# Kernel optimization log

Measured on AMD Instinct MI355X. Metric: run time of the kernel, lower is better.

The kernel has to match this reference:

```python
import jax, jax.numpy as jnp
import numpy as np
import math

B, WIN, C_IN, C_OUT = 8, 512, 38, 38
D_MODEL, N_HEADS, E_LAYERS, D_FF = 512, 8, 3, 512
EH = D_MODEL // N_HEADS
LN_EPS = 1e-3  # keras LayerNormalization default


def setup_inputs() -> dict:
    key = jax.random.key(0)
    ks = jax.random.split(key, 24)
    s = 0.02
    rn = lambda k, sh: jax.random.normal(k, sh, jnp.float32) * s
    L, d, H = E_LAYERS, D_MODEL, N_HEADS
    return {
        "x": jax.random.normal(ks[0], (B, WIN, C_IN), jnp.float32),
        "conv_k": rn(ks[1], (3, C_IN, d)),
        "Wq": rn(ks[2], (L, d, d)), "bq": jnp.zeros((L, d), jnp.float32),
        "Wk": rn(ks[3], (L, d, d)), "bk": jnp.zeros((L, d), jnp.float32),
        "Wv": rn(ks[4], (L, d, d)), "bv": jnp.zeros((L, d), jnp.float32),
        "Ws": rn(ks[5], (L, d, H)), "bs": jnp.zeros((L, H), jnp.float32),
        "Wo": rn(ks[6], (L, d, d)), "bo": jnp.zeros((L, d), jnp.float32),
        "W1": rn(ks[7], (L, d, D_FF)), "b1": jnp.zeros((L, D_FF), jnp.float32),
        "W2": rn(ks[8], (L, D_FF, d)), "b2": jnp.zeros((L, d), jnp.float32),
        "ln1_g": jnp.ones((L, d), jnp.float32), "ln1_b": jnp.zeros((L, d), jnp.float32),
        "ln2_g": jnp.ones((L, d), jnp.float32), "ln2_b": jnp.zeros((L, d), jnp.float32),
        "lnf_g": jnp.ones((d,), jnp.float32), "lnf_b": jnp.zeros((d,), jnp.float32),
        "Wp": rn(ks[9], (d, C_OUT)), "bp": jnp.zeros((C_OUT,), jnp.float32),
    }


def _layernorm(x, g, b):
    mu = jnp.mean(x, axis=-1, keepdims=True)
    var = jnp.mean((x - mu) ** 2, axis=-1, keepdims=True)
    return (x - mu) * jax.lax.rsqrt(var + LN_EPS) * g + b


def _pos_embedding():
    pos = jnp.arange(WIN, dtype=jnp.float32)[:, None]
    div = jnp.exp(jnp.arange(0, D_MODEL, 2, dtype=jnp.float32) * (-math.log(10000.0) / D_MODEL))
    # interleave sin at even idx, cos at odd idx
    return jnp.stack([jnp.sin(pos * div), jnp.cos(pos * div)], axis=-1).reshape(WIN, D_MODEL)


def reference(x, conv_k, Wq, bq, Wk, bk, Wv, bv, Ws, bs, Wo, bo,
              W1, b1, W2, b2, ln1_g, ln1_b, ln2_g, ln2_b, lnf_g, lnf_b, Wp, bp):
    # --- DataEmbedding: wrap-pad then Conv1D(k=3, valid), plus sinusoidal PE ---
    xp = jnp.concatenate([x[:, -1:], x, x[:, :1]], axis=1)
    h = jax.lax.conv_general_dilated(xp, conv_k, window_strides=(1,), padding='VALID',
                                     dimension_numbers=('NWC', 'WIO', 'NWC'))
    h = h + _pos_embedding()[None]

    idx = jnp.arange(WIN, dtype=jnp.float32)
    dist = jnp.abs(idx[:, None] - idx[None, :])
    scale = 1.0 / math.sqrt(EH)
    inv_sqrt_2pi = 1.0 / math.sqrt(2.0 * math.pi)

    series_l, prior_l, sigma_l = [], [], []
    for i in range(E_LAYERS):
        q = (h @ Wq[i] + bq[i]).reshape(B, WIN, N_HEADS, EH)
        k = (h @ Wk[i] + bk[i]).reshape(B, WIN, N_HEADS, EH)
        v = (h @ Wv[i] + bv[i]).reshape(B, WIN, N_HEADS, EH)
        sig = h @ Ws[i] + bs[i]

        scores = jnp.einsum('blhe,bshe->bhls', q, k)  # mask_flag=False in model
        series = jax.nn.softmax(scores * scale, axis=-1)  # [B, H, L, S]

        sg = jnp.transpose(sig, (0, 2, 1))               # [B, H, L]
        sg = jax.nn.sigmoid(sg * 5.0) + 1e-5
        sg = jnp.power(3.0, sg) - 1.0
        sg4 = jnp.broadcast_to(sg[..., None], (B, N_HEADS, WIN, WIN))
        prior = inv_sqrt_2pi / sg4 * jnp.exp(-(dist ** 2) / (2.0 * sg4 ** 2))

        attn_out = jnp.einsum('bhls,bshd->blhd', series, v).reshape(B, WIN, D_MODEL)
        h = _layernorm(h + attn_out @ Wo[i] + bo[i], ln1_g[i], ln1_b[i])
        y = jax.nn.gelu(h @ W1[i] + b1[i], approximate=False)
        y = y @ W2[i] + b2[i]
        h = _layernorm(h + y, ln2_g[i], ln2_b[i])

        series_l.append(series); prior_l.append(prior); sigma_l.append(sg4)

    h = _layernorm(h, lnf_g, lnf_b)
    out = h @ Wp + bp
    return (out, jnp.stack(series_l), jnp.stack(prior_l), jnp.stack(sigma_l))
```

## Files before the change

kernel.cpp:

```cpp
#include <hip/hip_runtime.h>
#include <math.h>


typedef unsigned short ushort;
typedef __attribute__((ext_vector_type(8))) ushort ushort8;
typedef __attribute__((ext_vector_type(8))) short short8;
typedef __attribute__((ext_vector_type(4))) float float4v;

__device__ inline ushort f2bf(float f) {
  union { float f; unsigned u; } v; v.f = f;
  return (ushort)((v.u + 0x7fffu + ((v.u >> 16) & 1u)) >> 16);
}

__global__ __launch_bounds__(512) void embed_kernel(const float* __restrict__ x,
                                                    const float* __restrict__ ck,
                                                    float* __restrict__ h) {
  int bt = blockIdx.x;
  int b = bt >> 9, t = bt & 511;
  int co = threadIdx.x;
  __shared__ float xs[3][38];
  if (co < 114) {
    int w = co / 38, ci = co - w * 38;
    int r = (t - 1 + w + 512) & 511;
    xs[w][ci] = x[((long)(b << 9) + r) * 38 + ci];
  }
  __syncthreads();
  float acc = 0.f;
#pragma unroll
  for (int w = 0; w < 3; ++w)
#pragma unroll
    for (int ci = 0; ci < 38; ++ci)
      acc = fmaf(xs[w][ci], ck[(w * 38 + ci) * 512 + co], acc);
  float div = expf((float)(co & ~1) * (-9.210340371976184f / 512.f));
  float ang = (float)t * div;
  float pe = (co & 1) ? cosf(ang) : sinf(ang);
  h[(long)bt * 512 + co] = acc + pe;
}

__global__ __launch_bounds__(256) void wcvt_kernel(const float* __restrict__ W,
                                                   ushort* __restrict__ Wt) {
  int l = blockIdx.z;
  int n = blockIdx.x * 256 + threadIdx.x;
  int k0 = blockIdx.y * 8;
  const float* w = W + (long)l * 262144;
  ushort* o = Wt + (long)l * 262144;
  ushort8 v;
#pragma unroll
  for (int i = 0; i < 8; ++i) v[i] = f2bf(w[(long)(k0 + i) * 512 + n]);
  *(ushort8*)&o[(long)n * 512 + k0] = v;
}

template <bool ABF16, bool BKMAJOR, bool GELU_, bool CBF16>
__global__ __launch_bounds__(256) void gemm_mfma(
    const void* __restrict__ Av, int lda, long sA1, long sA2,
    const ushort* __restrict__ B, int ldb, long sB1, long sB2,
    const float* __restrict__ bias,
    void* __restrict__ Cv, int ldc, long sC1, long sC2,
    int K, int bdiv, float alpha) {
  int z = blockIdx.z;
  int z1 = z / bdiv, z2 = z - z1 * bdiv;
  long aoff = (long)z1 * sA1 + (long)z2 * sA2;
  B += (long)z1 * sB1 + (long)z2 * sB2;
  long coff = (long)z1 * sC1 + (long)z2 * sC2;

  __shared__ ushort As[64 * 40];
  __shared__ ushort Bs[64 * 40];
  int t = threadIdx.x;
  int m0 = blockIdx.y * 64, n0 = blockIdx.x * 64;
  int w = t >> 6, lane = t & 63;
  int wr = (w >> 1) * 32, wc = (w & 1) * 32;
  int fm = lane & 15, koff = (lane >> 4) * 8;

  float4v acc[2][2] = {{{0.f, 0.f, 0.f, 0.f}, {0.f, 0.f, 0.f, 0.f}},
                       {{0.f, 0.f, 0.f, 0.f}, {0.f, 0.f, 0.f, 0.f}}};

  int sm = t >> 2, skq = (t & 3) * 8;
  int bk = t >> 3, bnq = (t & 7) * 8;

  for (int k0 = 0; k0 < K; k0 += 32) {
    if (ABF16) {
      const ushort* Ab = (const ushort*)Av + aoff;
      *(ushort8*)&As[sm * 40 + skq] =
          *(const ushort8*)&Ab[(long)(m0 + sm) * lda + k0 + skq];
    } else {
      const float* Af = (const float*)Av + aoff;
      const float* ap = &Af[(long)(m0 + sm) * lda + k0 + skq];
      float4 x0 = *(const float4*)ap;
      float4 x1 = *(const float4*)(ap + 4);
      ushort8 v;
      v[0] = f2bf(x0.x); v[1] = f2bf(x0.y); v[2] = f2bf(x0.z); v[3] = f2bf(x0.w);
      v[4] = f2bf(x1.x); v[5] = f2bf(x1.y); v[6] = f2bf(x1.z); v[7] = f2bf(x1.w);
      *(ushort8*)&As[sm * 40 + skq] = v;
    }
    if (!BKMAJOR) {
      *(ushort8*)&Bs[sm * 40 + skq] =
          *(const ushort8*)&B[(long)(n0 + sm) * ldb + k0 + skq];
    } else {
      ushort8 v = *(const ushort8*)&B[(long)(k0 + bk) * ldb + n0 + bnq];
#pragma unroll
      for (int i = 0; i < 8; ++i) Bs[(bnq + i) * 40 + bk] = v[i];
    }
    __syncthreads();

    short8 a0 = *(const short8*)&As[(wr + fm) * 40 + koff];
    short8 a1 = *(const short8*)&As[(wr + 16 + fm) * 40 + koff];
    short8 b0 = *(const short8*)&Bs[(wc + fm) * 40 + koff];
    short8 b1 = *(const short8*)&Bs[(wc + 16 + fm) * 40 + koff];
    acc[0][0] = __builtin_amdgcn_mfma_f32_16x16x32_bf16(a0, b0, acc[0][0], 0, 0, 0);
    acc[0][1] = __builtin_amdgcn_mfma_f32_16x16x32_bf16(a0, b1, acc[0][1], 0, 0, 0);
    acc[1][0] = __builtin_amdgcn_mfma_f32_16x16x32_bf16(a1, b0, acc[1][0], 0, 0, 0);
    acc[1][1] = __builtin_amdgcn_mfma_f32_16x16x32_bf16(a1, b1, acc[1][1], 0, 0, 0);
    __syncthreads();
  }

#pragma unroll
  for (int j = 0; j < 2; ++j) {
    int col = n0 + wc + 16 * j + fm;
    float bv = bias ? bias[col] : 0.f;
#pragma unroll
    for (int i = 0; i < 2; ++i) {
#pragma unroll
      for (int r = 0; r < 4; ++r) {
        int row = m0 + wr + 16 * i + (lane >> 4) * 4 + r;
        float v = acc[i][j][r] * alpha + bv;
        if (GELU_) v = 0.5f * v * (1.f + erff(v * 0.7071067811865476f));
        if (CBF16)
          ((ushort*)Cv)[coff + (long)row * ldc + col] = f2bf(v);
        else
          ((float*)Cv)[coff + (long)row * ldc + col] = v;
      }
    }
  }
}

__global__ __launch_bounds__(256) void softmax_kernel(float* __restrict__ P) {
  long row = (long)blockIdx.x * 4 + (threadIdx.x >> 6);
  int lane = threadIdx.x & 63;
  float* p = P + row * 512 + lane * 8;
  float4 v0 = *(float4*)p;
  float4 v1 = *(float4*)(p + 4);
  float m = fmaxf(fmaxf(fmaxf(v0.x, v0.y), fmaxf(v0.z, v0.w)),
                  fmaxf(fmaxf(v1.x, v1.y), fmaxf(v1.z, v1.w)));
#pragma unroll
  for (int off = 1; off < 64; off <<= 1) m = fmaxf(m, __shfl_xor(m, off));
  v0.x = __expf(v0.x - m); v0.y = __expf(v0.y - m);
  v0.z = __expf(v0.z - m); v0.w = __expf(v0.w - m);
  v1.x = __expf(v1.x - m); v1.y = __expf(v1.y - m);
  v1.z = __expf(v1.z - m); v1.w = __expf(v1.w - m);
  float s = v0.x + v0.y + v0.z + v0.w + v1.x + v1.y + v1.z + v1.w;
#pragma unroll
  for (int off = 1; off < 64; off <<= 1) s += __shfl_xor(s, off);
  float inv = 1.f / s;
  v0.x *= inv; v0.y *= inv; v0.z *= inv; v0.w *= inv;
  v1.x *= inv; v1.y *= inv; v1.z *= inv; v1.w *= inv;
  *(float4*)p = v0;
  *(float4*)(p + 4) = v1;
}

__global__ __launch_bounds__(256) void prior_kernel(const float* __restrict__ sig,
                                                    float* __restrict__ prior,
                                                    float* __restrict__ sigma4) {
  int blk = blockIdx.x;
  int i = blk & 511;
  int bh = blk >> 9;
  int b = bh >> 3, hh = bh & 7;
  float xv = sig[(((long)b << 9) + i) * 8 + hh];
  float s = 1.f / (1.f + expf(-5.f * xv)) + 1e-5f;
  float sg = expm1f(s * 1.0986122886681098f);
  float inv = 0.3989422804014327f / sg;
  float rinv = 1.f / sg;
  long base = ((long)bh << 18) + ((long)i << 9);
  int j0 = threadIdx.x * 2;
  float d0 = fabsf((float)(i - j0));
  float d1 = fabsf((float)(i - (j0 + 1)));
  float r0 = d0 * rinv, r1 = d1 * rinv;
  float2 pv = {inv * expf(-0.5f * r0 * r0), inv * expf(-0.5f * r1 * r1)};
  float2 sv = {sg, sg};
  *(float2*)&prior[base + j0] = pv;
  *(float2*)&sigma4[base + j0] = sv;
}

__global__ __launch_bounds__(256) void ln_kernel(const float* __restrict__ x,
                                                 const float* __restrict__ delta,
                                                 const float* __restrict__ g,
                                                 const float* __restrict__ bb,
                                                 float* __restrict__ out) {
  long row = blockIdx.x;
  int tid = threadIdx.x;
  int c = tid * 2;
  float2 xv = *(const float2*)&x[row * 512 + c];
  if (delta) {
    float2 dv = *(const float2*)&delta[row * 512 + c];
    xv.x += dv.x; xv.y += dv.y;
  }
  float s = xv.x + xv.y;
  float q = xv.x * xv.x + xv.y * xv.y;
#pragma unroll
  for (int off = 1; off < 64; off <<= 1) {
    s += __shfl_xor(s, off);
    q += __shfl_xor(q, off);
  }
  __shared__ float red[8];
  int wid = tid >> 6;
  if ((tid & 63) == 0) { red[wid] = s; red[wid + 4] = q; }
  __syncthreads();
  float S = red[0] + red[1] + red[2] + red[3];
  float Q = red[4] + red[5] + red[6] + red[7];
  float mean = S * (1.f / 512.f);
  float var = Q * (1.f / 512.f) - mean * mean;
  float rstd = rsqrtf(var + 1e-3f);
  float2 o;
  o.x = (xv.x - mean) * rstd * g[c] + bb[c];
  o.y = (xv.y - mean) * rstd * g[c + 1] + bb[c + 1];
  *(float2*)&out[row * 512 + c] = o;
}

template <int NOUT>
__global__ __launch_bounds__(256) void gemm_smallN(const float* __restrict__ A,
                                                   const float* __restrict__ W,
                                                   const float* __restrict__ bias,
                                                   float* __restrict__ C) {
  long row = (long)blockIdx.x * 4 + (threadIdx.x >> 6);
  int lane = threadIdx.x & 63;
  float acc[NOUT];
#pragma unroll
  for (int j = 0; j < NOUT; ++j) acc[j] = 0.f;
  for (int k = lane; k < 512; k += 64) {
    float a = A[row * 512 + k];
    const float* wr = W + (long)k * NOUT;
#pragma unroll
    for (int j = 0; j < NOUT; ++j) acc[j] = fmaf(a, wr[j], acc[j]);
  }
#pragma unroll
  for (int j = 0; j < NOUT; ++j)
#pragma unroll
    for (int off = 32; off; off >>= 1) acc[j] += __shfl_xor(acc[j], off);
  if (lane == 0) {
#pragma unroll
    for (int j = 0; j < NOUT; ++j) C[row * NOUT + j] = acc[j] + bias[j];
  }
}

extern "C" void kernel_launch(void* const* d_in, const int* in_sizes, int n_in,
                              void* d_out, int out_size, void* d_ws, size_t ws_size,
                              hipStream_t stream) {
  (void)in_sizes; (void)n_in; (void)out_size; (void)ws_size;
  const float* x    = (const float*)d_in[0];
  const float* ck   = (const float*)d_in[1];
  const float* Wq   = (const float*)d_in[2];
  const float* bq   = (const float*)d_in[3];
  const float* Wk   = (const float*)d_in[4];
  const float* bk   = (const float*)d_in[5];
  const float* Wv   = (const float*)d_in[6];
  const float* bv   = (const float*)d_in[7];
  const float* Wsw  = (const float*)d_in[8];
  const float* bsw  = (const float*)d_in[9];
  const float* Wo   = (const float*)d_in[10];
  const float* bo   = (const float*)d_in[11];
  const float* W1   = (const float*)d_in[12];
  const float* b1   = (const float*)d_in[13];
  const float* W2   = (const float*)d_in[14];
  const float* b2   = (const float*)d_in[15];
  const float* ln1g = (const float*)d_in[16];
  const float* ln1b = (const float*)d_in[17];
  const float* ln2g = (const float*)d_in[18];
  const float* ln2b = (const float*)d_in[19];
  const float* lnfg = (const float*)d_in[20];
  const float* lnfb = (const float*)d_in[21];
  const float* Wp   = (const float*)d_in[22];
  const float* bp   = (const float*)d_in[23];
  float* out = (float*)d_out;

  float* h  = (float*)d_ws;
  float* t1 = h + 2097152;
  float* t2 = t1 + 2097152;
  float* sg = t2 + 2097152;
  ushort* qb = (ushort*)(sg + 32768);
  ushort* kb = qb + 2097152;
  ushort* vb = kb + 2097152;
  ushort* wt = vb + 2097152;

  float* series0 = out + 155648;
  float* prior0  = out + 50487296;
  float* sigma0  = out + 100818944;

  dim3 gW(2, 64, 3);
  wcvt_kernel<<<gW, 256, 0, stream>>>(Wq, wt + 0L * 3 * 262144);
  wcvt_kernel<<<gW, 256, 0, stream>>>(Wk, wt + 1L * 3 * 262144);
  wcvt_kernel<<<gW, 256, 0, stream>>>(Wv, wt + 2L * 3 * 262144);
  wcvt_kernel<<<gW, 256, 0, stream>>>(Wo, wt + 3L * 3 * 262144);
  wcvt_kernel<<<gW, 256, 0, stream>>>(W1, wt + 4L * 3 * 262144);
  wcvt_kernel<<<gW, 256, 0, stream>>>(W2, wt + 5L * 3 * 262144);

  embed_kernel<<<4096, 512, 0, stream>>>(x, ck, h);

  dim3 gFull(8, 64, 1);
  dim3 gScore(8, 8, 64);
  dim3 gAttn(1, 8, 64);

  for (int l = 0; l < 3; ++l) {
    const ushort* wtq = wt + (0L * 3 + l) * 262144;
    const ushort* wtk = wt + (1L * 3 + l) * 262144;
    const ushort* wtv = wt + (2L * 3 + l) * 262144;
    const ushort* wto = wt + (3L * 3 + l) * 262144;
    const ushort* wt1 = wt + (4L * 3 + l) * 262144;
    const ushort* wt2 = wt + (5L * 3 + l) * 262144;
    const float* Ws_l = Wsw + (long)l * 4096;  const float* bs_l = bsw + (long)l * 8;
    float* ser = series0 + (long)l * 16777216;
    float* pri = prior0  + (long)l * 16777216;
    float* sgm = sigma0  + (long)l * 16777216;

    gemm_mfma<false, false, false, true><<<gFull, 256, 0, stream>>>(
        h, 512, 0, 0, wtq, 512, 0, 0, bq + (long)l * 512, qb, 512, 0, 0, 512, 1, 1.f);
    gemm_mfma<false, false, false, true><<<gFull, 256, 0, stream>>>(
        h, 512, 0, 0, wtk, 512, 0, 0, bk + (long)l * 512, kb, 512, 0, 0, 512, 1, 1.f);
    gemm_mfma<false, false, false, true><<<gFull, 256, 0, stream>>>(
        h, 512, 0, 0, wtv, 512, 0, 0, bv + (long)l * 512, vb, 512, 0, 0, 512, 1, 1.f);
    gemm_smallN<8><<<1024, 256, 0, stream>>>(h, Ws_l, bs_l, sg);
    gemm_mfma<true, false, false, false><<<gScore, 256, 0, stream>>>(
        qb, 512, 262144, 64, kb, 512, 262144, 64, nullptr,
        ser, 512, 2097152, 262144, 64, 8, 0.125f);
    softmax_kernel<<<8192, 256, 0, stream>>>(ser);
    prior_kernel<<<32768, 256, 0, stream>>>(sg, pri, sgm);
    gemm_mfma<false, true, false, false><<<gAttn, 256, 0, stream>>>(
        ser, 512, 2097152, 262144, vb, 512, 262144, 64, nullptr,
        t1, 512, 262144, 64, 512, 8, 1.f);
    gemm_mfma<false, false, false, false><<<gFull, 256, 0, stream>>>(
        t1, 512, 0, 0, wto, 512, 0, 0, bo + (long)l * 512, t2, 512, 0, 0, 512, 1, 1.f);
    ln_kernel<<<4096, 256, 0, stream>>>(h, t2, ln1g + l * 512, ln1b + l * 512, h);
    gemm_mfma<false, false, true, false><<<gFull, 256, 0, stream>>>(
        h, 512, 0, 0, wt1, 512, 0, 0, b1 + (long)l * 512, t1, 512, 0, 0, 512, 1, 1.f);
    gemm_mfma<false, false, false, false><<<gFull, 256, 0, stream>>>(
        t1, 512, 0, 0, wt2, 512, 0, 0, b2 + (long)l * 512, t2, 512, 0, 0, 512, 1, 1.f);
    ln_kernel<<<4096, 256, 0, stream>>>(h, t2, ln2g + l * 512, ln2b + l * 512, h);
  }

  ln_kernel<<<4096, 256, 0, stream>>>(h, nullptr, lnfg, lnfb, t1);
  gemm_smallN<38><<<1024, 256, 0, stream>>>(t1, Wp, bp, out);
}
```

Baseline: 1.244 ms.

## Fuse attention scores, softmax, PV and prior into one kernel; merge QKV GEMMs

Q, K and V projections now run as a single GEMM with concatenated weights and biases, writing an interleaved bf16 QKV buffer. A new fused attention kernel per 64-row tile and head computes scores with MFMA, does the row softmax in registers with cross-wave reductions, writes series, keeps the probabilities in LDS as bf16 for the PV product, and also writes prior and sigma. This removes the separate score, softmax, PV and prior launches and the re-reading of the large series matrix from global memory. The cost is heavy LDS use and a high register count at occupancy 1, and a serialized in-block prior write loop.

```diff
diff --git a/kernel.cpp b/kernel.cpp
--- a/kernel.cpp
+++ b/kernel.cpp
@@ -38,31 +38,36 @@
 }
 
 __global__ __launch_bounds__(256) void wcvt_kernel(const float* __restrict__ W,
-                                                   ushort* __restrict__ Wt) {
+                                                   ushort* __restrict__ Wt,
+                                                   long lstride) {
   int l = blockIdx.z;
   int n = blockIdx.x * 256 + threadIdx.x;
   int k0 = blockIdx.y * 8;
   const float* w = W + (long)l * 262144;
-  ushort* o = Wt + (long)l * 262144;
+  ushort* o = Wt + (long)l * lstride;
   ushort8 v;
 #pragma unroll
   for (int i = 0; i < 8; ++i) v[i] = f2bf(w[(long)(k0 + i) * 512 + n]);
   *(ushort8*)&o[(long)n * 512 + k0] = v;
 }
 
-template <bool ABF16, bool BKMAJOR, bool GELU_, bool CBF16>
+__global__ __launch_bounds__(512) void bcat_kernel(const float* __restrict__ bq,
+                                                   const float* __restrict__ bk,
+                                                   const float* __restrict__ bv,
+                                                   float* __restrict__ bqkv) {
+  int l = blockIdx.x, t = threadIdx.x;
+  bqkv[l * 1536 + t] = bq[l * 512 + t];
+  bqkv[l * 1536 + 512 + t] = bk[l * 512 + t];
+  bqkv[l * 1536 + 1024 + t] = bv[l * 512 + t];
+}
+
+template <bool ABF16, bool GELU_, bool CBF16>
 __global__ __launch_bounds__(256) void gemm_mfma(
-    const void* __restrict__ Av, int lda, long sA1, long sA2,
-    const ushort* __restrict__ B, int ldb, long sB1, long sB2,
+    const void* __restrict__ Av, int lda,
+    const ushort* __restrict__ B, int ldb,
     const float* __restrict__ bias,
-    void* __restrict__ Cv, int ldc, long sC1, long sC2,
-    int K, int bdiv, float alpha) {
-  int z = blockIdx.z;
-  int z1 = z / bdiv, z2 = z - z1 * bdiv;
-  long aoff = (long)z1 * sA1 + (long)z2 * sA2;
-  B += (long)z1 * sB1 + (long)z2 * sB2;
-  long coff = (long)z1 * sC1 + (long)z2 * sC2;
-
+    void* __restrict__ Cv, int ldc,
+    int K, float alpha) {
   __shared__ ushort As[64 * 40];
   __shared__ ushort Bs[64 * 40];
   int t = threadIdx.x;
@@ -73,17 +78,15 @@
 
   float4v acc[2][2] = {{{0.f, 0.f, 0.f, 0.f}, {0.f, 0.f, 0.f, 0.f}},
                        {{0.f, 0.f, 0.f, 0.f}, {0.f, 0.f, 0.f, 0.f}}};
-
   int sm = t >> 2, skq = (t & 3) * 8;
-  int bk = t >> 3, bnq = (t & 7) * 8;
 
   for (int k0 = 0; k0 < K; k0 += 32) {
     if (ABF16) {
-      const ushort* Ab = (const ushort*)Av + aoff;
+      const ushort* Ab = (const ushort*)Av;
       *(ushort8*)&As[sm * 40 + skq] =
           *(const ushort8*)&Ab[(long)(m0 + sm) * lda + k0 + skq];
     } else {
-      const float* Af = (const float*)Av + aoff;
+      const float* Af = (const float*)Av;
       const float* ap = &Af[(long)(m0 + sm) * lda + k0 + skq];
       float4 x0 = *(const float4*)ap;
       float4 x1 = *(const float4*)(ap + 4);
@@ -92,14 +95,8 @@
       v[4] = f2bf(x1.x); v[5] = f2bf(x1.y); v[6] = f2bf(x1.z); v[7] = f2bf(x1.w);
       *(ushort8*)&As[sm * 40 + skq] = v;
     }
-    if (!BKMAJOR) {
-      *(ushort8*)&Bs[sm * 40 + skq] =
-          *(const ushort8*)&B[(long)(n0 + sm) * ldb + k0 + skq];
-    } else {
-      ushort8 v = *(const ushort8*)&B[(long)(k0 + bk) * ldb + n0 + bnq];
-#pragma unroll
-      for (int i = 0; i < 8; ++i) Bs[(bnq + i) * 40 + bk] = v[i];
-    }
+    *(ushort8*)&Bs[sm * 40 + skq] =
+        *(const ushort8*)&B[(long)(n0 + sm) * ldb + k0 + skq];
     __syncthreads();
 
     short8 a0 = *(const short8*)&As[(wr + fm) * 40 + koff];
@@ -125,59 +122,213 @@
         float v = acc[i][j][r] * alpha + bv;
         if (GELU_) v = 0.5f * v * (1.f + erff(v * 0.7071067811865476f));
         if (CBF16)
-          ((ushort*)Cv)[coff + (long)row * ldc + col] = f2bf(v);
+          ((ushort*)Cv)[(long)row * ldc + col] = f2bf(v);
         else
-          ((float*)Cv)[coff + (long)row * ldc + col] = v;
+          ((float*)Cv)[(long)row * ldc + col] = v;
       }
     }
   }
 }
 
-__global__ __launch_bounds__(256) void softmax_kernel(float* __restrict__ P) {
-  long row = (long)blockIdx.x * 4 + (threadIdx.x >> 6);
-  int lane = threadIdx.x & 63;
-  float* p = P + row * 512 + lane * 8;
-  float4 v0 = *(float4*)p;
-  float4 v1 = *(float4*)(p + 4);
-  float m = fmaxf(fmaxf(fmaxf(v0.x, v0.y), fmaxf(v0.z, v0.w)),
-                  fmaxf(fmaxf(v1.x, v1.y), fmaxf(v1.z, v1.w)));
-#pragma unroll
-  for (int off = 1; off < 64; off <<= 1) m = fmaxf(m, __shfl_xor(m, off));
-  v0.x = __expf(v0.x - m); v0.y = __expf(v0.y - m);
-  v0.z = __expf(v0.z - m); v0.w = __expf(v0.w - m);
-  v1.x = __expf(v1.x - m); v1.y = __expf(v1.y - m);
-  v1.z = __expf(v1.z - m); v1.w = __expf(v1.w - m);
-  float s = v0.x + v0.y + v0.z + v0.w + v1.x + v1.y + v1.z + v1.w;
-#pragma unroll
-  for (int off = 1; off < 64; off <<= 1) s += __shfl_xor(s, off);
-  float inv = 1.f / s;
-  v0.x *= inv; v0.y *= inv; v0.z *= inv; v0.w *= inv;
-  v1.x *= inv; v1.y *= inv; v1.z *= inv; v1.w *= inv;
-  *(float4*)p = v0;
-  *(float4*)(p + 4) = v1;
-}
-
-__global__ __launch_bounds__(256) void prior_kernel(const float* __restrict__ sig,
-                                                    float* __restrict__ prior,
-                                                    float* __restrict__ sigma4) {
-  int blk = blockIdx.x;
-  int i = blk & 511;
-  int bh = blk >> 9;
+__global__ __launch_bounds__(256, 1) void attn_fused(
+    const ushort* __restrict__ qkv, const float* __restrict__ sg,
+    float* __restrict__ series, float* __restrict__ prior,
+    float* __restrict__ sigma, float* __restrict__ t1) {
+  __shared__ ushort KPs[36864];
+  __shared__ ushort Qs[4608];
+  __shared__ ushort Vc[4608];
+  __shared__ float red[256];
+
+  int t = threadIdx.x;
+  int m0 = blockIdx.x * 64;
+  int bh = blockIdx.y;
   int b = bh >> 3, hh = bh & 7;
-  float xv = sig[(((long)b << 9) + i) * 8 + hh];
-  float s = 1.f / (1.f + expf(-5.f * xv)) + 1e-5f;
-  float sg = expm1f(s * 1.0986122886681098f);
-  float inv = 0.3989422804014327f / sg;
-  float rinv = 1.f / sg;
-  long base = ((long)bh << 18) + ((long)i << 9);
-  int j0 = threadIdx.x * 2;
-  float d0 = fabsf((float)(i - j0));
-  float d1 = fabsf((float)(i - (j0 + 1)));
-  float r0 = d0 * rinv, r1 = d1 * rinv;
-  float2 pv = {inv * expf(-0.5f * r0 * r0), inv * expf(-0.5f * r1 * r1)};
-  float2 sv = {sg, sg};
-  *(float2*)&prior[base + j0] = pv;
-  *(float2*)&sigma4[base + j0] = sv;
+  int w = t >> 6, lane = t & 63;
+  int fm = lane & 15, q4 = lane >> 4;
+  int wc = w * 128;
+  long rowg = (long)b * 512;
+
+  {
+    int row = t >> 2, kq = (t & 3) * 16;
+    const ushort* src = &qkv[(rowg + m0 + row) * 1536 + hh * 64 + kq];
+    *(ushort8*)&Qs[row * 72 + kq] = *(const ushort8*)src;
+    *(ushort8*)&Qs[row * 72 + kq + 8] = *(const ushort8*)(src + 8);
+#pragma unroll
+    for (int p = 0; p < 8; ++p) {
+      int srow = p * 64 + row;
+      const ushort* ks = &qkv[(rowg + srow) * 1536 + 512 + hh * 64 + kq];
+      *(ushort8*)&KPs[srow * 72 + kq] = *(const ushort8*)ks;
+      *(ushort8*)&KPs[srow * 72 + kq + 8] = *(const ushort8*)(ks + 8);
+    }
+  }
+  __syncthreads();
+
+  float4v acc[4][8];
+#pragma unroll
+  for (int i = 0; i < 4; ++i)
+#pragma unroll
+    for (int j = 0; j < 8; ++j) acc[i][j] = (float4v){0.f, 0.f, 0.f, 0.f};
+
+#pragma unroll
+  for (int ks = 0; ks < 2; ++ks) {
+    int ko = ks * 32 + q4 * 8;
+    short8 a[4], bfr[8];
+#pragma unroll
+    for (int i = 0; i < 4; ++i)
+      a[i] = *(const short8*)&Qs[(16 * i + fm) * 72 + ko];
+#pragma unroll
+    for (int j = 0; j < 8; ++j)
+      bfr[j] = *(const short8*)&KPs[(wc + 16 * j + fm) * 72 + ko];
+#pragma unroll
+    for (int i = 0; i < 4; ++i)
+#pragma unroll
+      for (int j = 0; j < 8; ++j)
+        acc[i][j] = __builtin_amdgcn_mfma_f32_16x16x32_bf16(a[i], bfr[j], acc[i][j], 0, 0, 0);
+  }
+
+#pragma unroll
+  for (int i = 0; i < 4; ++i)
+#pragma unroll
+    for (int j = 0; j < 8; ++j)
+#pragma unroll
+      for (int r = 0; r < 4; ++r) acc[i][j][r] *= 0.125f;
+
+  float mrow[4][4];
+#pragma unroll
+  for (int i = 0; i < 4; ++i)
+#pragma unroll
+    for (int r = 0; r < 4; ++r) {
+      float m = acc[i][0][r];
+#pragma unroll
+      for (int j = 1; j < 8; ++j) m = fmaxf(m, acc[i][j][r]);
+#pragma unroll
+      for (int off = 1; off < 16; off <<= 1) m = fmaxf(m, __shfl_xor(m, off));
+      mrow[i][r] = m;
+    }
+  if (fm == 0) {
+#pragma unroll
+    for (int i = 0; i < 4; ++i)
+#pragma unroll
+      for (int r = 0; r < 4; ++r)
+        red[(16 * i + q4 * 4 + r) * 4 + w] = mrow[i][r];
+  }
+  __syncthreads();
+#pragma unroll
+  for (int i = 0; i < 4; ++i)
+#pragma unroll
+    for (int r = 0; r < 4; ++r) {
+      const float* rp = &red[(16 * i + q4 * 4 + r) * 4];
+      mrow[i][r] = fmaxf(fmaxf(rp[0], rp[1]), fmaxf(rp[2], rp[3]));
+    }
+  float lrow[4][4];
+#pragma unroll
+  for (int i = 0; i < 4; ++i)
+#pragma unroll
+    for (int r = 0; r < 4; ++r) {
+      float s = 0.f;
+#pragma unroll
+      for (int j = 0; j < 8; ++j) {
+        float e = __expf(acc[i][j][r] - mrow[i][r]);
+        acc[i][j][r] = e;
+        s += e;
+      }
+#pragma unroll
+      for (int off = 1; off < 16; off <<= 1) s += __shfl_xor(s, off);
+      lrow[i][r] = s;
+    }
+  __syncthreads();
+  if (fm == 0) {
+#pragma unroll
+    for (int i = 0; i < 4; ++i)
+#pragma unroll
+      for (int r = 0; r < 4; ++r)
+        red[(16 * i + q4 * 4 + r) * 4 + w] = lrow[i][r];
+  }
+  __syncthreads();
+#pragma unroll
+  for (int i = 0; i < 4; ++i)
+#pragma unroll
+    for (int r = 0; r < 4; ++r) {
+      const float* rp = &red[(16 * i + q4 * 4 + r) * 4];
+      lrow[i][r] = 1.f / (rp[0] + rp[1] + rp[2] + rp[3]);
+    }
+
+  float* serp = series + ((long)bh << 18);
+#pragma unroll
+  for (int i = 0; i < 4; ++i)
+#pragma unroll
+    for (int r = 0; r < 4; ++r) {
+      int row = 16 * i + q4 * 4 + r;
+      float inv = lrow[i][r];
+#pragma unroll
+      for (int j = 0; j < 8; ++j) {
+        int col = wc + 16 * j + fm;
+        float v = acc[i][j][r] * inv;
+        serp[(long)(m0 + row) * 512 + col] = v;
+        KPs[row * 520 + col] = f2bf(v);
+      }
+    }
+
+  float4v acc2[4] = {{0.f, 0.f, 0.f, 0.f}, {0.f, 0.f, 0.f, 0.f},
+                     {0.f, 0.f, 0.f, 0.f}, {0.f, 0.f, 0.f, 0.f}};
+  int wn = w * 16;
+  int s_local = t >> 2, cgrp = (t & 3) * 16;
+  for (int c = 0; c < 8; ++c) {
+    __syncthreads();
+    const ushort* vs = &qkv[(rowg + c * 64 + s_local) * 1536 + 1024 + hh * 64 + cgrp];
+    ushort8 v0 = *(const ushort8*)vs;
+    ushort8 v1 = *(const ushort8*)(vs + 8);
+#pragma unroll
+    for (int e = 0; e < 8; ++e) {
+      Vc[(cgrp + e) * 72 + s_local] = v0[e];
+      Vc[(cgrp + 8 + e) * 72 + s_local] = v1[e];
+    }
+    __syncthreads();
+#pragma unroll
+    for (int ks = 0; ks < 2; ++ks) {
+      int ko = ks * 32 + q4 * 8;
+      short8 b2 = *(const short8*)&Vc[(wn + fm) * 72 + ko];
+#pragma unroll
+      for (int i = 0; i < 4; ++i) {
+        short8 a2 = *(const short8*)&KPs[(16 * i + fm) * 520 + c * 64 + ko];
+        acc2[i] = __builtin_amdgcn_mfma_f32_16x16x32_bf16(a2, b2, acc2[i], 0, 0, 0);
+      }
+    }
+  }
+#pragma unroll
+  for (int i = 0; i < 4; ++i)
+#pragma unroll
+    for (int r = 0; r < 4; ++r)
+      t1[(rowg + m0 + 16 * i + q4 * 4 + r) * 512 + hh * 64 + wn + fm] = acc2[i][r];
+
+  __syncthreads();
+  if (t < 64) {
+    float xv = sg[(rowg + m0 + t) * 8 + hh];
+    float s = 1.f / (1.f + __expf(-5.f * xv)) + 1e-5f;
+    float sgv = expm1f(s * 1.0986122886681098f);
+    red[t * 3] = sgv;
+    red[t * 3 + 1] = 0.3989422804014327f / sgv;
+    red[t * 3 + 2] = 1.f / sgv;
+  }
+  __syncthreads();
+  float* prip = prior + ((long)bh << 18);
+  float* sigp = sigma + ((long)bh << 18);
+  for (int it = t; it < 8192; it += 256) {
+    int row = it >> 7;
+    int c4 = (it & 127) << 2;
+    float sgv = red[row * 3], inv = red[row * 3 + 1], rinv = red[row * 3 + 2];
+    float ig = (float)(m0 + row);
+    float4 pv, sv;
+#pragma unroll
+    for (int e = 0; e < 4; ++e) {
+      float dd = ig - (float)(c4 + e);
+      float rr = dd * rinv;
+      ((float*)&pv)[e] = inv * __expf(-0.5f * rr * rr);
+      ((float*)&sv)[e] = sgv;
+    }
+    *(float4*)&prip[(long)(m0 + row) * 512 + c4] = pv;
+    *(float4*)&sigp[(long)(m0 + row) * 512 + c4] = sv;
+  }
 }
 
 __global__ __launch_bounds__(256) void ln_kernel(const float* __restrict__ x,
@@ -271,67 +422,52 @@
   const float* bp   = (const float*)d_in[23];
   float* out = (float*)d_out;
 
-  float* h  = (float*)d_ws;
-  float* t1 = h + 2097152;
-  float* t2 = t1 + 2097152;
-  float* sg = t2 + 2097152;
-  ushort* qb = (ushort*)(sg + 32768);
-  ushort* kb = qb + 2097152;
-  ushort* vb = kb + 2097152;
-  ushort* wt = vb + 2097152;
+  float* h    = (float*)d_ws;
+  float* t1   = h + 2097152;
+  float* t2   = t1 + 2097152;
+  float* sg   = t2 + 2097152;
+  float* bqkv = sg + 32768;
+  ushort* qkv  = (ushort*)(bqkv + 4608);
+  ushort* wqkv = qkv + 6291456;
+  ushort* wo3  = wqkv + 2359296;
+  ushort* w13  = wo3 + 786432;
+  ushort* w23  = w13 + 786432;
 
   float* series0 = out + 155648;
   float* prior0  = out + 50487296;
   float* sigma0  = out + 100818944;
 
   dim3 gW(2, 64, 3);
-  wcvt_kernel<<<gW, 256, 0, stream>>>(Wq, wt + 0L * 3 * 262144);
-  wcvt_kernel<<<gW, 256, 0, stream>>>(Wk, wt + 1L * 3 * 262144);
-  wcvt_kernel<<<gW, 256, 0, stream>>>(Wv, wt + 2L * 3 * 262144);
-  wcvt_kernel<<<gW, 256, 0, stream>>>(Wo, wt + 3L * 3 * 262144);
-  wcvt_kernel<<<gW, 256, 0, stream>>>(W1, wt + 4L * 3 * 262144);
-  wcvt_kernel<<<gW, 256, 0, stream>>>(W2, wt + 5L * 3 * 262144);
+  wcvt_kernel<<<gW, 256, 0, stream>>>(Wq, wqkv, 786432);
+  wcvt_kernel<<<gW, 256, 0, stream>>>(Wk, wqkv + 262144, 786432);
+  wcvt_kernel<<<gW, 256, 0, stream>>>(Wv, wqkv + 524288, 786432);
+  wcvt_kernel<<<gW, 256, 0, stream>>>(Wo, wo3, 262144);
+  wcvt_kernel<<<gW, 256, 0, stream>>>(W1, w13, 262144);
+  wcvt_kernel<<<gW, 256, 0, stream>>>(W2, w23, 262144);
+  bcat_kernel<<<3, 512, 0, stream>>>(bq, bk, bv, bqkv);
 
   embed_kernel<<<4096, 512, 0, stream>>>(x, ck, h);
 
+  dim3 gQKV(24, 64, 1);
   dim3 gFull(8, 64, 1);
-  dim3 gScore(8, 8, 64);
-  dim3 gAttn(1, 8, 64);
+  dim3 gAttn(8, 64, 1);
 
   for (int l = 0; l < 3; ++l) {
-    const ushort* wtq = wt + (0L * 3 + l) * 262144;
-    const ushort* wtk = wt + (1L * 3 + l) * 262144;
-    const ushort* wtv = wt + (2L * 3 + l) * 262144;
-    const ushort* wto = wt + (3L * 3 + l) * 262144;
-    const ushort* wt1 = wt + (4L * 3 + l) * 262144;
-    const ushort* wt2 = wt + (5L * 3 + l) * 262144;
-    const float* Ws_l = Wsw + (long)l * 4096;  const float* bs_l = bsw + (long)l * 8;
     float* ser = series0 + (long)l * 16777216;
     float* pri = prior0  + (long)l * 16777216;
     float* sgm = sigma0  + (long)l * 16777216;
 
-    gemm_mfma<false, false, false, true><<<gFull, 256, 0, stream>>>(
-        h, 512, 0, 0, wtq, 512, 0, 0, bq + (long)l * 512, qb, 512, 0, 0, 512, 1, 1.f);
-    gemm_mfma<false, false, false, true><<<gFull, 256, 0, stream>>>(
-        h, 512, 0, 0, wtk, 512, 0, 0, bk + (long)l * 512, kb, 512, 0, 0, 512, 1, 1.f);
-    gemm_mfma<false, false, false, true><<<gFull, 256, 0, stream>>>(
-        h, 512, 0, 0, wtv, 512, 0, 0, bv + (long)l * 512, vb, 512, 0, 0, 512, 1, 1.f);
-    gemm_smallN<8><<<1024, 256, 0, stream>>>(h, Ws_l, bs_l, sg);
-    gemm_mfma<true, false, false, false><<<gScore, 256, 0, stream>>>(
-        qb, 512, 262144, 64, kb, 512, 262144, 64, nullptr,
-        ser, 512, 2097152, 262144, 64, 8, 0.125f);
-    softmax_kernel<<<8192, 256, 0, stream>>>(ser);
-    prior_kernel<<<32768, 256, 0, stream>>>(sg, pri, sgm);
-    gemm_mfma<false, true, false, false><<<gAttn, 256, 0, stream>>>(
-        ser, 512, 2097152, 262144, vb, 512, 262144, 64, nullptr,
-        t1, 512, 262144, 64, 512, 8, 1.f);
-    gemm_mfma<false, false, false, false><<<gFull, 256, 0, stream>>>(
-        t1, 512, 0, 0, wto, 512, 0, 0, bo + (long)l * 512, t2, 512, 0, 0, 512, 1, 1.f);
+    gemm_mfma<false, false, true><<<gQKV, 256, 0, stream>>>(
+        h, 512, wqkv + (long)l * 786432, 512, bqkv + l * 1536, qkv, 1536, 512, 1.f);
+    gemm_smallN<8><<<1024, 256, 0, stream>>>(h, Wsw + (long)l * 4096, bsw + l * 8, sg);
+    attn_fused<<<gAttn, 256, 0, stream>>>(qkv, sg, ser, pri, sgm, t1);
+    gemm_mfma<false, false, false><<<gFull, 256, 0, stream>>>(
+        t1, 512, wo3 + (long)l * 262144, 512, bo + (long)l * 512, t2, 512, 512, 1.f);
     ln_kernel<<<4096, 256, 0, stream>>>(h, t2, ln1g + l * 512, ln1b + l * 512, h);
-    gemm_mfma<false, false, true, false><<<gFull, 256, 0, stream>>>(
-        h, 512, 0, 0, wt1, 512, 0, 0, b1 + (long)l * 512, t1, 512, 0, 0, 512, 1, 1.f);
-    gemm_mfma<false, false, false, false><<<gFull, 256, 0, stream>>>(
-        t1, 512, 0, 0, wt2, 512, 0, 0, b2 + (long)l * 512, t2, 512, 0, 0, 512, 1, 1.f);
+    gemm_mfma<false, true, false><<<gFull, 256, 0, stream>>>(
+        h, 512, w13 + (long)l * 262144, 512, b1 + (long)l * 512, t1, 512, 512, 1.f);
+    gemm_mfma<false, false, false><<<gFull, 256, 0, stream>>>(
+        t1, 512, w23 + (long)l * 262144, 512, b2 + (long)l * 512, t2, 512, 512, 1.f);
     ln_kernel<<<4096, 256, 0, stream>>>(h, t2, ln2g + l * 512, ln2b + l * 512, h);
   }
 
```

Result: faster. 1.083 ms (-13.0%).
